# Kernel tuning notes

Hardware: AMD Instinct MI355X
Metric: run time of the kernel (lower is better)

The kernel has to match this reference:

```python
import jax, jax.numpy as jnp
import numpy as np

TEMPERATURE = 0.07
SIM_THRESHOLD = 0.5


def setup_inputs() -> dict:
    key = jax.random.key(0)
    k1, k2 = jax.random.split(key)
    features = jax.random.normal(k1, (4096, 2, 128), dtype=jnp.float32)
    labels = jax.random.randint(k2, (4096, 100), 0, 2).astype(jnp.float32)
    return {"features": features, "labels": labels}


def reference(features, labels):
    B, V, D = features.shape

    # label Jaccard similarity -> positive/negative masks [B, B]
    intersection = labels @ labels.T
    row_sum = jnp.sum(labels, axis=1, keepdims=True)
    union = row_sum + row_sum.T - intersection
    similarity = intersection / (union + 1e-6)
    positive_mask = (similarity >= SIM_THRESHOLD).astype(jnp.float32)
    negative_mask = 1.0 - positive_mask

    # torch.cat(torch.unbind(features, dim=1), dim=0) -> [V*B, D] (view-major)
    contrast_feature = jnp.transpose(features, (1, 0, 2)).reshape(V * B, D)
    dot_similarities = (contrast_feature @ contrast_feature.T) / TEMPERATURE  # [VB, VB]

    # numerical stability: subtract detached row max over the FULL row
    logits_max = jax.lax.stop_gradient(jnp.max(dot_similarities, axis=1, keepdims=True))
    logits = dot_similarities - logits_max

    # only the top-left [B, B] block is ever indexed by the original loop
    e = jnp.exp(logits[:B, :B])
    pos_sum = jnp.sum(e * positive_mask, axis=1)  # [B]
    neg_sum = jnp.sum(e * negative_mask, axis=1)  # [B]

    has_pos = jnp.sum(positive_mask, axis=1) > 0  # rows with >=1 positive
    pos_safe = jnp.where(has_pos, pos_sum, 1.0)
    den_safe = jnp.where(has_pos, pos_sum + neg_sum, 1.0)
    per_row = -jnp.log(pos_safe / den_safe)

    count = jnp.sum(has_pos.astype(jnp.float32))
    loss = jnp.sum(jnp.where(has_pos, per_row, 0.0)) / jnp.maximum(count, 1.0)
    return loss
```

## Files before the change

### kernel.cpp

```cpp
#include <hip/hip_runtime.h>
#include <math.h>

#define B_ROWS 4096
#define LBL 100
#define NCT 32
#define NTRI 528

typedef __attribute__((ext_vector_type(8))) short bf16x8;
typedef __attribute__((ext_vector_type(4))) float f32x4;

__device__ __forceinline__ unsigned f2bf(float x) {
  union { float f; unsigned u; } a; a.f = x;
  unsigned r = a.u + 0x7fffu + ((a.u >> 16) & 1u);
  return r >> 16;
}

__device__ __forceinline__ void lds_dma16(void* l, const void* g) {
  __builtin_amdgcn_global_load_lds(
      (const __attribute__((address_space(1))) void*)g,
      (__attribute__((address_space(3))) void*)l, 16, 0, 0);
}

__global__ void pack_kernel(const float* __restrict__ feat,
                            uint4* __restrict__ cf) {
  int g = blockIdx.x * 256 + threadIdx.x;
  int tile = g >> 11, rem = g & 2047;
  int r = rem >> 4, kc = rem & 15;
  const float* src = feat + ((size_t)(tile * 128 + r)) * 256 + kc * 8;
  float4 a = *(const float4*)src;
  float4 b = *(const float4*)(src + 4);
  uint4 ov;
  ov.x = f2bf(a.x) | (f2bf(a.y) << 16);
  ov.y = f2bf(a.z) | (f2bf(a.w) << 16);
  ov.z = f2bf(b.x) | (f2bf(b.y) << 16);
  ov.w = f2bf(b.z) | (f2bf(b.w) << 16);
  cf[(size_t)tile * 2048 + kc * 128 + (r ^ kc)] = ov;
}

__global__ void seedlabel_kernel(const float* __restrict__ feat,
                                 const float* __restrict__ labels,
                                 uint4* __restrict__ Lb,
                                 int* __restrict__ rsv,
                                 float* __restrict__ seedRaw,
                                 float* __restrict__ accum) {
  if (blockIdx.x == 0 && threadIdx.x < 2) accum[threadIdx.x] = 0.0f;
  int w = (int)((blockIdx.x * blockDim.x + threadIdx.x) >> 6);
  int lane = threadIdx.x & 63;
  const float2* src = (const float2*)(feat + (size_t)w * 256);
  float2 f = src[lane];
  float b0 = __uint_as_float(f2bf(f.x) << 16);
  float b1 = __uint_as_float(f2bf(f.y) << 16);
  float s = b0 * b0 + b1 * b1;
  #pragma unroll
  for (int o = 32; o >= 1; o >>= 1) s += __shfl_xor(s, o);
  float x0 = labels[(size_t)w * LBL + lane];
  float x1 = (lane < LBL - 64) ? labels[(size_t)w * LBL + 64 + lane] : 0.0f;
  unsigned long long m0 = __ballot(x0 != 0.0f);
  unsigned long long m1 = __ballot(x1 != 0.0f);
  if (lane == 0) {
    Lb[w] = make_uint4((unsigned)m0, (unsigned)(m0 >> 32),
                       (unsigned)m1, (unsigned)(m1 >> 32));
    rsv[w] = __popcll(m0) + __popcll(m1);
    seedRaw[w] = s - 0.15f;
  }
}

__launch_bounds__(256, 2)
__global__ void main_kernel(const uint4* __restrict__ cf,
                            const uint4* __restrict__ Lb,
                            const int* __restrict__ rsv,
                            const float* __restrict__ seedRaw,
                            float2* __restrict__ part) {
  __shared__ uint4 As[2048];
  __shared__ uint4 Bs[2048];
  __shared__ uint4 rLbS[128], cLbS[128];
  __shared__ int rRsS[128], cRsS[128];
  __shared__ float sS[128], sB[128];

  int bid = blockIdx.x;
  int bx = 0, off = 0;
  while (bid >= off + (NCT - bx)) { off += NCT - bx; ++bx; }
  int by = bx + (bid - off);
  const bool diag = (bx == by);

  const int tid = threadIdx.x;
  const int lane = tid & 63;
  const int l15 = lane & 15;
  const int quad = lane >> 4;
  const int wave = tid >> 6;
  const int wi = (wave & 1) * 64;
  const int wj = (wave >> 1) * 64;
  const int rowBase = bx * 128;
  const int colBase = by * 128;
  const float invT = 1.0f / 0.07f;

  #pragma unroll
  for (int it = 0; it < 8; ++it) {
    int flat = it * 256 + tid;
    lds_dma16(&As[flat], &cf[(size_t)bx * 2048 + flat]);
    lds_dma16(&Bs[flat], &cf[(size_t)by * 2048 + flat]);
  }
  if (tid < 128) {
    cLbS[tid] = Lb[colBase + tid];
    cRsS[tid] = rsv[colBase + tid];
    sB[tid] = seedRaw[colBase + tid];
  } else {
    int t = tid - 128;
    rLbS[t] = Lb[rowBase + t];
    rRsS[t] = rsv[rowBase + t];
    sS[t] = seedRaw[rowBase + t];
  }
  __syncthreads();

  float srow[16], scol[4];
  #pragma unroll
  for (int ti = 0; ti < 4; ++ti)
    #pragma unroll
    for (int r = 0; r < 4; ++r)
      srow[ti * 4 + r] = sS[wi + ti * 16 + quad * 4 + r];
  #pragma unroll
  for (int tj = 0; tj < 4; ++tj) scol[tj] = sB[wj + tj * 16 + l15];

  const bf16x8* Asv = (const bf16x8*)As;
  const bf16x8* Bsv = (const bf16x8*)Bs;

  f32x4 acc[4][4];
  #pragma unroll
  for (int ti = 0; ti < 4; ++ti)
    #pragma unroll
    for (int tj = 0; tj < 4; ++tj)
      acc[ti][tj] = (f32x4){0.f, 0.f, 0.f, 0.f};

  #pragma unroll
  for (int ks = 0; ks < 4; ++ks) {
    const int kc = ks * 4 + quad;
    const int abase = kc * 128 + wi + (l15 ^ kc);
    const int bbase = kc * 128 + wj + (l15 ^ kc);
    bf16x8 af[4], bfr[4];
    #pragma unroll
    for (int t = 0; t < 4; ++t) {
      af[t] = Asv[abase + t * 16];
      bfr[t] = Bsv[bbase + t * 16];
    }
    #pragma unroll
    for (int ti = 0; ti < 4; ++ti)
      #pragma unroll
      for (int tj = 0; tj < 4; ++tj)
        acc[ti][tj] = __builtin_amdgcn_mfma_f32_16x16x32_bf16(
            af[ti], bfr[tj], acc[ti][tj], 0, 0, 0);
  }

  float p_s[16], n_s[16], cp[4], cn[4], cmax[4];
  #pragma unroll
  for (int i = 0; i < 16; ++i) { p_s[i] = 0.f; n_s[i] = 0.f; }
  #pragma unroll
  for (int tj = 0; tj < 4; ++tj) { cp[tj] = 0.f; cn[tj] = 0.f; cmax[tj] = -1e30f; }

  #pragma unroll
  for (int ti = 0; ti < 4; ++ti)
    #pragma unroll
    for (int r = 0; r < 4; ++r) {
      int si = ti * 4 + r;
      float l0 = acc[ti][0][r], l1 = acc[ti][1][r];
      float l2 = acc[ti][2][r], l3 = acc[ti][3][r];
      cmax[0] = fmaxf(cmax[0], l0);
      cmax[1] = fmaxf(cmax[1], l1);
      cmax[2] = fmaxf(cmax[2], l2);
      cmax[3] = fmaxf(cmax[3], l3);
      float tm = fmaxf(fmaxf(l0, l1), fmaxf(l2, l3));
      if (tm > srow[si] - 6.3f) {
        int lrow = wi + ti * 16 + quad * 4 + r;
        uint4 la = rLbS[lrow];
        int ra = rRsS[lrow];
        float p = p_s[si], n = n_s[si];
        float lv[4] = {l0, l1, l2, l3};
        #pragma unroll
        for (int tj = 0; tj < 4; ++tj) {
          float e = __expf((lv[tj] - srow[si]) * invT);
          int lcol = wj + tj * 16 + l15;
          uint4 lb = cLbS[lcol];
          int inter = __popc(la.x & lb.x) + __popc(la.y & lb.y) +
                      __popc(la.z & lb.z) + __popc(la.w & lb.w);
          if (3 * inter > ra + cRsS[lcol]) p += e; else n += e;
        }
        p_s[si] = p;
        n_s[si] = n;
      }
    }

  if (!diag) {
    #pragma unroll
    for (int tj = 0; tj < 4; ++tj) {
      if (cmax[tj] > scol[tj] - 6.3f) {
        int lcol = wj + tj * 16 + l15;
        uint4 lb = cLbS[lcol];
        int rb = cRsS[lcol];
        float p = cp[tj], n = cn[tj];
        #pragma unroll
        for (int ti = 0; ti < 4; ++ti)
          #pragma unroll
          for (int r = 0; r < 4; ++r) {
            float e = __expf((acc[ti][tj][r] - scol[tj]) * invT);
            int lrow = wi + ti * 16 + quad * 4 + r;
            uint4 la = rLbS[lrow];
            int inter = __popc(la.x & lb.x) + __popc(la.y & lb.y) +
                        __popc(la.z & lb.z) + __popc(la.w & lb.w);
            if (3 * inter > rRsS[lrow] + rb) p += e; else n += e;
          }
        cp[tj] = p;
        cn[tj] = n;
      }
    }
  }

  #pragma unroll
  for (int si = 0; si < 16; ++si) {
    float p = p_s[si], n = n_s[si];
    #pragma unroll
    for (int o = 8; o >= 1; o >>= 1) {
      p += __shfl_xor(p, o);
      n += __shfl_xor(n, o);
    }
    p_s[si] = p;
    n_s[si] = n;
  }
  #pragma unroll
  for (int tj = 0; tj < 4; ++tj) {
    float p = cp[tj], n = cn[tj];
    p += __shfl_xor(p, 16); n += __shfl_xor(n, 16);
    p += __shfl_xor(p, 32); n += __shfl_xor(n, 32);
    cp[tj] = p;
    cn[tj] = n;
  }

  __syncthreads();
  float* mrow = (float*)As;
  float* mcol = ((float*)As) + 256;
  if (wj == 64 && l15 == 0) {
    #pragma unroll
    for (int ti = 0; ti < 4; ++ti)
      #pragma unroll
      for (int r = 0; r < 4; ++r) {
        int row = wi + ti * 16 + quad * 4 + r;
        int si = ti * 4 + r;
        mrow[row * 2 + 0] = p_s[si];
        mrow[row * 2 + 1] = n_s[si];
      }
  }
  if (!diag && wi == 64 && quad == 0) {
    #pragma unroll
    for (int tj = 0; tj < 4; ++tj) {
      int col = wj + tj * 16 + l15;
      mcol[col * 2 + 0] = cp[tj];
      mcol[col * 2 + 1] = cn[tj];
    }
  }
  __syncthreads();
  if (wj == 0 && l15 == 0) {
    #pragma unroll
    for (int ti = 0; ti < 4; ++ti)
      #pragma unroll
      for (int r = 0; r < 4; ++r) {
        int row = wi + ti * 16 + quad * 4 + r;
        int si = ti * 4 + r;
        float p = p_s[si] + mrow[row * 2 + 0];
        float n = n_s[si] + mrow[row * 2 + 1];
        part[(size_t)by * B_ROWS + rowBase + row] = make_float2(p, n);
      }
  }
  if (!diag && wi == 0 && quad == 0) {
    #pragma unroll
    for (int tj = 0; tj < 4; ++tj) {
      int col = wj + tj * 16 + l15;
      float p = cp[tj] + mcol[col * 2 + 0];
      float n = cn[tj] + mcol[col * 2 + 1];
      part[(size_t)bx * B_ROWS + colBase + col] = make_float2(p, n);
    }
  }
}

__global__ void merge_kernel(const float2* __restrict__ part,
                             const int* __restrict__ rsv,
                             float* __restrict__ accum) {
  int row = blockIdx.x * 256 + threadIdx.x;
  float p = 0.f, n = 0.f;
  #pragma unroll
  for (int c = 0; c < NCT; ++c) {
    float2 v = part[(size_t)c * B_ROWS + row];
    p += v.x;
    n += v.y;
  }
  float per = 0.f, cnt = 0.f;
  if (rsv[row] > 0) {
    per = -logf(p / (p + n));
    cnt = 1.f;
  }
  #pragma unroll
  for (int o = 32; o >= 1; o >>= 1) {
    per += __shfl_xor(per, o);
    cnt += __shfl_xor(cnt, o);
  }
  if ((threadIdx.x & 63) == 0) {
    atomicAdd(accum + 0, per);
    atomicAdd(accum + 1, cnt);
  }
}

__global__ void fin_kernel(const float* __restrict__ accum,
                           float* __restrict__ out) {
  out[0] = accum[0] / fmaxf(accum[1], 1.0f);
}

extern "C" void kernel_launch(void* const* d_in, const int* in_sizes, int n_in,
                              void* d_out, int out_size, void* d_ws, size_t ws_size,
                              hipStream_t stream) {
  const float* feat = (const float*)d_in[0];
  const float* labels = (const float*)d_in[1];
  float* out = (float*)d_out;
  char* ws = (char*)d_ws;
  uint4* cf = (uint4*)(ws + 0);
  uint4* Lbm = (uint4*)(ws + 1048576);
  int* rsv = (int*)(ws + 1114112);
  float* seedRaw = (float*)(ws + 1130496);
  float2* part = (float2*)(ws + 1146880);
  float* accum = (float*)(ws + 1146880 + 1048576);

  hipLaunchKernelGGL(pack_kernel, dim3(256), dim3(256), 0, stream, feat, cf);
  hipLaunchKernelGGL(seedlabel_kernel, dim3(1024), dim3(256), 0, stream,
                     feat, labels, Lbm, rsv, seedRaw, accum);
  hipLaunchKernelGGL(main_kernel, dim3(NTRI), dim3(256), 0, stream,
                     cf, Lbm, rsv, seedRaw, part);
  hipLaunchKernelGGL(merge_kernel, dim3(B_ROWS / 256), dim3(256), 0, stream,
                     part, rsv, accum);
  hipLaunchKernelGGL(fin_kernel, dim3(1), dim3(1), 0, stream, accum, out);
}
```

Measured before the change: 83.31 us.

## Fuse prep and finalize kernels, drop LDS staging in main tile kernel

Pack and seed/label work are merged into one prep kernel, with the bf16 packing done through wave shuffles. The finalize step moves into the merge kernel, where a last-block atomic counter writes the result, so two kernel launches go away. The main kernel no longer stages tiles and label data in shared memory. It reads MFMA fragments straight from global memory with a one-step register prefetch, and it writes per-half-tile partials instead of reducing them through LDS barriers. This removes LDS use and syncthreads, and the relaxed launch bounds may allow higher occupancy. In exchange it adds uncached global reads of label bitmasks inside the hot loop, doubles the partials the merge must read, and may raise register pressure.

```diff
diff --git a/kernel.cpp b/kernel.cpp
--- a/kernel.cpp
+++ b/kernel.cpp
@@ -14,42 +14,26 @@
   unsigned r = a.u + 0x7fffu + ((a.u >> 16) & 1u);
   return r >> 16;
 }
-
-__device__ __forceinline__ void lds_dma16(void* l, const void* g) {
-  __builtin_amdgcn_global_load_lds(
-      (const __attribute__((address_space(1))) void*)g,
-      (__attribute__((address_space(3))) void*)l, 16, 0, 0);
-}
-
-__global__ void pack_kernel(const float* __restrict__ feat,
-                            uint4* __restrict__ cf) {
-  int g = blockIdx.x * 256 + threadIdx.x;
-  int tile = g >> 11, rem = g & 2047;
-  int r = rem >> 4, kc = rem & 15;
-  const float* src = feat + ((size_t)(tile * 128 + r)) * 256 + kc * 8;
-  float4 a = *(const float4*)src;
-  float4 b = *(const float4*)(src + 4);
-  uint4 ov;
-  ov.x = f2bf(a.x) | (f2bf(a.y) << 16);
-  ov.y = f2bf(a.z) | (f2bf(a.w) << 16);
-  ov.z = f2bf(b.x) | (f2bf(b.y) << 16);
-  ov.w = f2bf(b.z) | (f2bf(b.w) << 16);
-  cf[(size_t)tile * 2048 + kc * 128 + (r ^ kc)] = ov;
-}
-
-__global__ void seedlabel_kernel(const float* __restrict__ feat,
-                                 const float* __restrict__ labels,
-                                 uint4* __restrict__ Lb,
-                                 int* __restrict__ rsv,
-                                 float* __restrict__ seedRaw,
-                                 float* __restrict__ accum) {
+__device__ __forceinline__ float bf2f(unsigned h) {
+  return __uint_as_float(h << 16);
+}
+
+__global__ void prep_kernel(const float* __restrict__ feat,
+                            const float* __restrict__ labels,
+                            uint4* __restrict__ cf,
+                            uint4* __restrict__ Lb,
+                            int* __restrict__ rsv,
+                            float* __restrict__ seedRaw,
+                            float* __restrict__ accum,
+                            unsigned* __restrict__ counter) {
   if (blockIdx.x == 0 && threadIdx.x < 2) accum[threadIdx.x] = 0.0f;
-  int w = (int)((blockIdx.x * blockDim.x + threadIdx.x) >> 6);
+  if (blockIdx.x == 0 && threadIdx.x == 2) *counter = 0u;
+  int w = blockIdx.x * 4 + (threadIdx.x >> 6);
   int lane = threadIdx.x & 63;
-  const float2* src = (const float2*)(feat + (size_t)w * 256);
-  float2 f = src[lane];
-  float b0 = __uint_as_float(f2bf(f.x) << 16);
-  float b1 = __uint_as_float(f2bf(f.y) << 16);
+  float2 f = ((const float2*)(feat + (size_t)w * 256))[lane];
+  unsigned u0 = f2bf(f.x), u1 = f2bf(f.y);
+  unsigned myu = u0 | (u1 << 16);
+  float b0 = bf2f(u0), b1 = bf2f(u1);
   float s = b0 * b0 + b1 * b1;
   #pragma unroll
   for (int o = 32; o >= 1; o >>= 1) s += __shfl_xor(s, o);
@@ -57,6 +41,14 @@
   float x1 = (lane < LBL - 64) ? labels[(size_t)w * LBL + 64 + lane] : 0.0f;
   unsigned long long m0 = __ballot(x0 != 0.0f);
   unsigned long long m1 = __ballot(x1 != 0.0f);
+  int kc = lane & 15;
+  unsigned q0 = __shfl(myu, kc * 4 + 0);
+  unsigned q1 = __shfl(myu, kc * 4 + 1);
+  unsigned q2 = __shfl(myu, kc * 4 + 2);
+  unsigned q3 = __shfl(myu, kc * 4 + 3);
+  if (lane < 16)
+    cf[(size_t)(w >> 7) * 2048 + kc * 128 + ((w & 127) ^ kc)] =
+        make_uint4(q0, q1, q2, q3);
   if (lane == 0) {
     Lb[w] = make_uint4((unsigned)m0, (unsigned)(m0 >> 32),
                        (unsigned)m1, (unsigned)(m1 >> 32));
@@ -65,18 +57,12 @@
   }
 }
 
-__launch_bounds__(256, 2)
+__launch_bounds__(256)
 __global__ void main_kernel(const uint4* __restrict__ cf,
                             const uint4* __restrict__ Lb,
                             const int* __restrict__ rsv,
                             const float* __restrict__ seedRaw,
-                            float2* __restrict__ part) {
-  __shared__ uint4 As[2048];
-  __shared__ uint4 Bs[2048];
-  __shared__ uint4 rLbS[128], cLbS[128];
-  __shared__ int rRsS[128], cRsS[128];
-  __shared__ float sS[128], sB[128];
-
+                            float2* __restrict__ part2) {
   int bid = blockIdx.x;
   int bx = 0, off = 0;
   while (bid >= off + (NCT - bx)) { off += NCT - bx; ++bx; }
@@ -94,35 +80,8 @@
   const int colBase = by * 128;
   const float invT = 1.0f / 0.07f;
 
-  #pragma unroll
-  for (int it = 0; it < 8; ++it) {
-    int flat = it * 256 + tid;
-    lds_dma16(&As[flat], &cf[(size_t)bx * 2048 + flat]);
-    lds_dma16(&Bs[flat], &cf[(size_t)by * 2048 + flat]);
-  }
-  if (tid < 128) {
-    cLbS[tid] = Lb[colBase + tid];
-    cRsS[tid] = rsv[colBase + tid];
-    sB[tid] = seedRaw[colBase + tid];
-  } else {
-    int t = tid - 128;
-    rLbS[t] = Lb[rowBase + t];
-    rRsS[t] = rsv[rowBase + t];
-    sS[t] = seedRaw[rowBase + t];
-  }
-  __syncthreads();
-
-  float srow[16], scol[4];
-  #pragma unroll
-  for (int ti = 0; ti < 4; ++ti)
-    #pragma unroll
-    for (int r = 0; r < 4; ++r)
-      srow[ti * 4 + r] = sS[wi + ti * 16 + quad * 4 + r];
-  #pragma unroll
-  for (int tj = 0; tj < 4; ++tj) scol[tj] = sB[wj + tj * 16 + l15];
-
-  const bf16x8* Asv = (const bf16x8*)As;
-  const bf16x8* Bsv = (const bf16x8*)Bs;
+  const uint4* Ab = cf + (size_t)bx * 2048;
+  const uint4* Bb = cf + (size_t)by * 2048;
 
   f32x4 acc[4][4];
   #pragma unroll
@@ -131,16 +90,24 @@
     for (int tj = 0; tj < 4; ++tj)
       acc[ti][tj] = (f32x4){0.f, 0.f, 0.f, 0.f};
 
+  bf16x8 af[4], bfr[4], af2[4], bfr2[4];
+  {
+    const int kc = quad;
+    #pragma unroll
+    for (int t = 0; t < 4; ++t) {
+      af[t]  = *(const bf16x8*)&Ab[kc * 128 + ((wi + t * 16 + l15) ^ kc)];
+      bfr[t] = *(const bf16x8*)&Bb[kc * 128 + ((wj + t * 16 + l15) ^ kc)];
+    }
+  }
   #pragma unroll
   for (int ks = 0; ks < 4; ++ks) {
-    const int kc = ks * 4 + quad;
-    const int abase = kc * 128 + wi + (l15 ^ kc);
-    const int bbase = kc * 128 + wj + (l15 ^ kc);
-    bf16x8 af[4], bfr[4];
-    #pragma unroll
-    for (int t = 0; t < 4; ++t) {
-      af[t] = Asv[abase + t * 16];
-      bfr[t] = Bsv[bbase + t * 16];
+    if (ks < 3) {
+      const int kc = (ks + 1) * 4 + quad;
+      #pragma unroll
+      for (int t = 0; t < 4; ++t) {
+        af2[t]  = *(const bf16x8*)&Ab[kc * 128 + ((wi + t * 16 + l15) ^ kc)];
+        bfr2[t] = *(const bf16x8*)&Bb[kc * 128 + ((wj + t * 16 + l15) ^ kc)];
+      }
     }
     #pragma unroll
     for (int ti = 0; ti < 4; ++ti)
@@ -148,6 +115,27 @@
       for (int tj = 0; tj < 4; ++tj)
         acc[ti][tj] = __builtin_amdgcn_mfma_f32_16x16x32_bf16(
             af[ti], bfr[tj], acc[ti][tj], 0, 0, 0);
+    if (ks < 3) {
+      #pragma unroll
+      for (int t = 0; t < 4; ++t) { af[t] = af2[t]; bfr[t] = bfr2[t]; }
+    }
+  }
+
+  uint4 clb[4];
+  int crs[4];
+  float scol[4], srow[16];
+  #pragma unroll
+  for (int tj = 0; tj < 4; ++tj) {
+    int gcol = colBase + wj + tj * 16 + l15;
+    clb[tj] = Lb[gcol];
+    crs[tj] = rsv[gcol];
+    scol[tj] = seedRaw[gcol];
+  }
+  #pragma unroll
+  for (int ti = 0; ti < 4; ++ti) {
+    float4 s4 = *(const float4*)&seedRaw[rowBase + wi + ti * 16 + quad * 4];
+    srow[ti * 4 + 0] = s4.x; srow[ti * 4 + 1] = s4.y;
+    srow[ti * 4 + 2] = s4.z; srow[ti * 4 + 3] = s4.w;
   }
 
   float p_s[16], n_s[16], cp[4], cn[4], cmax[4];
@@ -169,19 +157,17 @@
       cmax[3] = fmaxf(cmax[3], l3);
       float tm = fmaxf(fmaxf(l0, l1), fmaxf(l2, l3));
       if (tm > srow[si] - 6.3f) {
-        int lrow = wi + ti * 16 + quad * 4 + r;
-        uint4 la = rLbS[lrow];
-        int ra = rRsS[lrow];
+        int grow = rowBase + wi + ti * 16 + quad * 4 + r;
+        uint4 la = Lb[grow];
+        int ra = rsv[grow];
         float p = p_s[si], n = n_s[si];
         float lv[4] = {l0, l1, l2, l3};
         #pragma unroll
         for (int tj = 0; tj < 4; ++tj) {
           float e = __expf((lv[tj] - srow[si]) * invT);
-          int lcol = wj + tj * 16 + l15;
-          uint4 lb = cLbS[lcol];
-          int inter = __popc(la.x & lb.x) + __popc(la.y & lb.y) +
-                      __popc(la.z & lb.z) + __popc(la.w & lb.w);
-          if (3 * inter > ra + cRsS[lcol]) p += e; else n += e;
+          int inter = __popc(la.x & clb[tj].x) + __popc(la.y & clb[tj].y) +
+                      __popc(la.z & clb[tj].z) + __popc(la.w & clb[tj].w);
+          if (3 * inter > ra + crs[tj]) p += e; else n += e;
         }
         p_s[si] = p;
         n_s[si] = n;
@@ -192,20 +178,17 @@
     #pragma unroll
     for (int tj = 0; tj < 4; ++tj) {
       if (cmax[tj] > scol[tj] - 6.3f) {
-        int lcol = wj + tj * 16 + l15;
-        uint4 lb = cLbS[lcol];
-        int rb = cRsS[lcol];
         float p = cp[tj], n = cn[tj];
         #pragma unroll
         for (int ti = 0; ti < 4; ++ti)
           #pragma unroll
           for (int r = 0; r < 4; ++r) {
             float e = __expf((acc[ti][tj][r] - scol[tj]) * invT);
-            int lrow = wi + ti * 16 + quad * 4 + r;
-            uint4 la = rLbS[lrow];
-            int inter = __popc(la.x & lb.x) + __popc(la.y & lb.y) +
-                        __popc(la.z & lb.z) + __popc(la.w & lb.w);
-            if (3 * inter > rRsS[lrow] + rb) p += e; else n += e;
+            int grow = rowBase + wi + ti * 16 + quad * 4 + r;
+            uint4 la = Lb[grow];
+            int inter = __popc(la.x & clb[tj].x) + __popc(la.y & clb[tj].y) +
+                        __popc(la.z & clb[tj].z) + __popc(la.w & clb[tj].w);
+            if (3 * inter > rsv[grow] + crs[tj]) p += e; else n += e;
           }
         cp[tj] = p;
         cn[tj] = n;
@@ -223,6 +206,17 @@
     }
     p_s[si] = p;
     n_s[si] = n;
+  }
+  if (l15 == 0) {
+    int sc = by * 2 + (wj >> 6);
+    #pragma unroll
+    for (int ti = 0; ti < 4; ++ti)
+      #pragma unroll
+      for (int r = 0; r < 4; ++r) {
+        int row = rowBase + wi + ti * 16 + quad * 4 + r;
+        part2[(size_t)sc * B_ROWS + row] =
+            make_float2(p_s[ti * 4 + r], n_s[ti * 4 + r]);
+      }
   }
   #pragma unroll
   for (int tj = 0; tj < 4; ++tj) {
@@ -232,61 +226,26 @@
     cp[tj] = p;
     cn[tj] = n;
   }
-
-  __syncthreads();
-  float* mrow = (float*)As;
-  float* mcol = ((float*)As) + 256;
-  if (wj == 64 && l15 == 0) {
-    #pragma unroll
-    for (int ti = 0; ti < 4; ++ti)
-      #pragma unroll
-      for (int r = 0; r < 4; ++r) {
-        int row = wi + ti * 16 + quad * 4 + r;
-        int si = ti * 4 + r;
-        mrow[row * 2 + 0] = p_s[si];
-        mrow[row * 2 + 1] = n_s[si];
-      }
-  }
-  if (!diag && wi == 64 && quad == 0) {
+  if (!diag && quad == 0) {
+    int sc = bx * 2 + (wi >> 6);
     #pragma unroll
     for (int tj = 0; tj < 4; ++tj) {
-      int col = wj + tj * 16 + l15;
-      mcol[col * 2 + 0] = cp[tj];
-      mcol[col * 2 + 1] = cn[tj];
-    }
-  }
-  __syncthreads();
-  if (wj == 0 && l15 == 0) {
-    #pragma unroll
-    for (int ti = 0; ti < 4; ++ti)
-      #pragma unroll
-      for (int r = 0; r < 4; ++r) {
-        int row = wi + ti * 16 + quad * 4 + r;
-        int si = ti * 4 + r;
-        float p = p_s[si] + mrow[row * 2 + 0];
-        float n = n_s[si] + mrow[row * 2 + 1];
-        part[(size_t)by * B_ROWS + rowBase + row] = make_float2(p, n);
-      }
-  }
-  if (!diag && wi == 0 && quad == 0) {
-    #pragma unroll
-    for (int tj = 0; tj < 4; ++tj) {
-      int col = wj + tj * 16 + l15;
-      float p = cp[tj] + mcol[col * 2 + 0];
-      float n = cn[tj] + mcol[col * 2 + 1];
-      part[(size_t)bx * B_ROWS + colBase + col] = make_float2(p, n);
-    }
-  }
-}
-
-__global__ void merge_kernel(const float2* __restrict__ part,
-                             const int* __restrict__ rsv,
-                             float* __restrict__ accum) {
+      int col = colBase + wj + tj * 16 + l15;
+      part2[(size_t)sc * B_ROWS + col] = make_float2(cp[tj], cn[tj]);
+    }
+  }
+}
+
+__global__ void mergefin_kernel(const float2* __restrict__ part2,
+                                const int* __restrict__ rsv,
+                                float* __restrict__ accum,
+                                unsigned* __restrict__ counter,
+                                float* __restrict__ out) {
   int row = blockIdx.x * 256 + threadIdx.x;
   float p = 0.f, n = 0.f;
   #pragma unroll
-  for (int c = 0; c < NCT; ++c) {
-    float2 v = part[(size_t)c * B_ROWS + row];
+  for (int c = 0; c < 2 * NCT; ++c) {
+    float2 v = part2[(size_t)c * B_ROWS + row];
     p += v.x;
     n += v.y;
   }
@@ -304,11 +263,17 @@
     atomicAdd(accum + 0, per);
     atomicAdd(accum + 1, cnt);
   }
-}
-
-__global__ void fin_kernel(const float* __restrict__ accum,
-                           float* __restrict__ out) {
-  out[0] = accum[0] / fmaxf(accum[1], 1.0f);
+  __syncthreads();
+  __threadfence();
+  __shared__ unsigned done;
+  if (threadIdx.x == 0) done = atomicAdd(counter, 1u);
+  __syncthreads();
+  if (done == 15 && threadIdx.x == 0) {
+    __threadfence();
+    float P = atomicAdd(accum + 0, 0.0f);
+    float C = atomicAdd(accum + 1, 0.0f);
+    out[0] = P / fmaxf(C, 1.0f);
+  }
 }
 
 extern "C" void kernel_launch(void* const* d_in, const int* in_sizes, int n_in,
@@ -322,15 +287,14 @@
   uint4* Lbm = (uint4*)(ws + 1048576);
   int* rsv = (int*)(ws + 1114112);
   float* seedRaw = (float*)(ws + 1130496);
-  float2* part = (float2*)(ws + 1146880);
-  float* accum = (float*)(ws + 1146880 + 1048576);
-
-  hipLaunchKernelGGL(pack_kernel, dim3(256), dim3(256), 0, stream, feat, cf);
-  hipLaunchKernelGGL(seedlabel_kernel, dim3(1024), dim3(256), 0, stream,
-                     feat, labels, Lbm, rsv, seedRaw, accum);
+  float2* part2 = (float2*)(ws + 1146880);
+  float* accum = (float*)(ws + 1146880 + 2097152);
+  unsigned* counter = (unsigned*)(ws + 1146880 + 2097152 + 8);
+
+  hipLaunchKernelGGL(prep_kernel, dim3(1024), dim3(256), 0, stream,
+                     feat, labels, cf, Lbm, rsv, seedRaw, accum, counter);
   hipLaunchKernelGGL(main_kernel, dim3(NTRI), dim3(256), 0, stream,
-                     cf, Lbm, rsv, seedRaw, part);
-  hipLaunchKernelGGL(merge_kernel, dim3(B_ROWS / 256), dim3(256), 0, stream,
-                     part, rsv, accum);
-  hipLaunchKernelGGL(fin_kernel, dim3(1), dim3(1), 0, stream, accum, out);
-}
+                     cf, Lbm, rsv, seedRaw, part2);
+  hipLaunchKernelGGL(mergefin_kernel, dim3(B_ROWS / 256), dim3(256), 0, stream,
+                     part2, rsv, accum, counter, out);
+}
```

Result: no change. 82.67 us (-0.8%).
